# Performance work log

Hardware: AMD Instinct MI355X
Metric: run time of the kernel (lower is better)

## Reference

```python
import jax, jax.numpy as jnp
import numpy as np

N = 50000      # num nodes
E = 300000     # num edges
C = 256        # channels
H = 8          # num_heads
DH = C // H    # head_dim = 32
NUM_DST = 256  # dst indices live in [0, NUM_DST) -> anchor columns of BFS frontier
MAX_SPD = 3
EPS = 1e-5     # LayerNorm eps (torch default)


def setup_inputs() -> dict:
    key = jax.random.key(0)
    ks = jax.random.split(key, 10)
    scale = 1.0 / np.sqrt(C).astype(np.float32)
    x = jax.random.normal(ks[0], (N, C), jnp.float32)
    src = jax.random.randint(ks[1], (E,), 0, N, dtype=jnp.int32)
    dst = jax.random.randint(ks[2], (E,), 0, NUM_DST, dtype=jnp.int32)
    Wq = jax.random.normal(ks[3], (C, C), jnp.float32) * scale
    Wk = jax.random.normal(ks[4], (C, C), jnp.float32) * scale
    Wv = jax.random.normal(ks[5], (C, C), jnp.float32) * scale
    bq = jax.random.normal(ks[6], (C,), jnp.float32) * scale
    bk = jax.random.normal(ks[7], (C,), jnp.float32) * scale
    bv = jax.random.normal(ks[8], (C,), jnp.float32) * scale
    spd_w = jax.random.normal(ks[9], (MAX_SPD + 2, H), jnp.float32)
    gamma = jnp.ones((C,), jnp.float32)
    beta = jnp.zeros((C,), jnp.float32)
    return dict(x=x, src=src, dst=dst, Wq=Wq, bq=bq, Wk=Wk, bk=bk,
                Wv=Wv, bv=bv, spd_w=spd_w, gamma=gamma, beta=beta)


def _spd_buckets(src, dst):
    # Reverse-BFS shortest-path buckets (use_reverse=True, directed):
    # A[row=dst, col=src]; F_k = bin(A @ F_{k-1}); anchors are dst nodes,
    # which all live in [0, NUM_DST) so the anchor->column map is identity.
    row, col = dst, src
    F = (jnp.arange(N)[:, None] == jnp.arange(NUM_DST)[None, :]).astype(jnp.float32)  # [N, M]
    spd = jnp.full((E,), MAX_SPD + 1, jnp.int32)
    unset = jnp.ones((E,), bool)
    for k in range(1, MAX_SPD + 1):
        # (A @ F)[i] = sum over edges with row==i of F[col]
        F = (jax.ops.segment_sum(F[col], row, num_segments=N) > 0).astype(jnp.float32)
        reach = F[src, dst] > 0
        newly = unset & reach
        spd = jnp.where(newly, k, spd)
        unset = unset & ~newly
    return spd


def _segment_softmax(scores, seg, n):
    # numerically stable softmax over edges grouped by destination node
    m = jax.ops.segment_max(scores, seg, num_segments=n)
    ex = jnp.exp(scores - m[seg])
    s = jax.ops.segment_sum(ex, seg, num_segments=n)
    return ex / s[seg]


def reference(x, src, dst, Wq, bq, Wk, bk, Wv, bv, spd_w, gamma, beta):
    Q = (x @ Wq.T + bq).reshape(N, H, DH)
    K = (x @ Wk.T + bk).reshape(N, H, DH)
    V = (x @ Wv.T + bv).reshape(N, H, DH)
    # per-edge dot-product scores [E, H]
    scores = (Q[dst] * K[src]).sum(-1) / np.float32(np.sqrt(DH))
    spd = jax.lax.stop_gradient(_spd_buckets(src, dst))  # torch.no_grad
    scores = scores + spd_w[spd]
    w = _segment_softmax(scores, dst, N)  # [E, H] (dropout is identity in eval)
    msg = (V[src] * w[:, :, None]).reshape(E, C)
    out = jax.ops.segment_sum(msg, dst, num_segments=N)  # scatter-add aggregation
    # total degree (in + out) broadcast over channels
    ones_e = jnp.ones((E,), jnp.float32)
    deg = jax.ops.segment_sum(ones_e, src, num_segments=N) + \
          jax.ops.segment_sum(ones_e, dst, num_segments=N)
    h = out + deg[:, None] + x  # residual
    mu = h.mean(-1, keepdims=True)
    var = ((h - mu) ** 2).mean(-1, keepdims=True)
    return (h - mu) / jnp.sqrt(var + EPS) * gamma + beta
```

## Files before the change

### kernel.cpp

```cpp
#include <hip/hip_runtime.h>
#include <stdint.h>

#define N_NODES 50000
#define E_EDGES 300000
#define C_CH    256
#define H_HEADS 8
#define NB2     64
#define CHUNK2  4688
#define NBIN    4096
#define SRCDIV  3125
#define NWG_GEMM 2346
#define NWG_LN   12436

typedef unsigned short u16;
typedef unsigned int   u32;

typedef __attribute__((ext_vector_type(8))) short  v8s;
typedef __attribute__((ext_vector_type(4))) float  v4f;

__device__ __forceinline__ float bf2f(u16 v) {
    union { u32 u; float f; } x; x.u = ((u32)v) << 16; return x.f;
}
__device__ __forceinline__ u16 f2bf(float f) {
    union { float f; u32 u; } x; x.f = f;
    u32 r = (x.u + 0x7FFFu + ((x.u >> 16) & 1u)) >> 16;
    return (u16)r;
}
__device__ __forceinline__ void unp2(u32 v, float& lo, float& hi) {
    union { u32 u; float f; } x;
    x.u = v << 16; lo = x.f;
    x.u = v & 0xFFFF0000u; hi = x.f;
}
__device__ __forceinline__ void gl_lds16(const u16* g, u16* l) {
    __builtin_amdgcn_global_load_lds(
        (const __attribute__((address_space(1))) void*)g,
        (__attribute__((address_space(3))) void*)l, 16, 0, 0);
}
__device__ __forceinline__ void pack8(const float4 p, const float4 q, u16* dst) {
    u16 tmp[8];
    tmp[0]=f2bf(p.x); tmp[1]=f2bf(p.y); tmp[2]=f2bf(p.z); tmp[3]=f2bf(p.w);
    tmp[4]=f2bf(q.x); tmp[5]=f2bf(q.y); tmp[6]=f2bf(q.z); tmp[7]=f2bf(q.w);
    *(uint4*)dst = *(const uint4*)tmp;
}

__global__ __launch_bounds__(256) void prep_k(
    const float* __restrict__ Wk, const float* __restrict__ Wv,
    const float* __restrict__ Wq, u16* __restrict__ Wb,
    const int* __restrict__ src, const int* __restrict__ dst,
    u32* __restrict__ blockhist, u32* __restrict__ bintot,
    u32* __restrict__ inmask)
{
    __shared__ u32 hist[NBIN];
    int t = threadIdx.x, b = blockIdx.x;
    if (b < 192) {
        int m = (b < 64) ? 0 : (b < 128) ? 1 : 2;
        const float* sp = (m == 0) ? Wk : (m == 1) ? Wv : Wq;
        u16* dp = Wb + m * 65536;
        int i = (b & 63) * 1024 + t * 4;
        float4 v = *(const float4*)(sp + i);
        ushort4 o;
        o.x = f2bf(v.x); o.y = f2bf(v.y); o.z = f2bf(v.z); o.w = f2bf(v.w);
        *(ushort4*)(dp + i) = o;
        return;
    }
    int hb = b - 192;
#pragma unroll
    for (int j = 0; j < 16; j++) hist[t + j * 256] = 0;
    __syncthreads();
    int start = hb * CHUNK2;
    int end = start + CHUNK2; if (end > E_EDGES) end = E_EDGES;
    for (int e = start + t; e < end; e += 256) {
        int d = dst[e], s = src[e];
        atomicAdd(&hist[d * 16 + s / SRCDIV], 1u);
        if (s < 256) atomicOr(&inmask[d * 8 + (s >> 5)], 1u << (s & 31));
    }
    __syncthreads();
#pragma unroll
    for (int j = 0; j < 16; j++) {
        int bin = t + j * 256;
        u32 h = hist[bin];
        blockhist[hb * NBIN + bin] = h;
        if (h) atomicAdd(&bintot[bin], h);
    }
}

__global__ __launch_bounds__(256, 4) void gemm3(
    const float* __restrict__ x, const u16* __restrict__ Wb,
    const float* __restrict__ bk, const float* __restrict__ bv,
    const float* __restrict__ bq,
    u16* __restrict__ Kb, u16* __restrict__ Vb, u16* __restrict__ Qb,
    const u32* __restrict__ bintot, u32* __restrict__ bin_off,
    const u32* __restrict__ inmask, unsigned char* __restrict__ T,
    const float* __restrict__ gamma, const float* __restrict__ beta,
    float* __restrict__ y)
{
    __shared__ u16 smem[4][128 * 32];
    const int t = threadIdx.x;

    if (blockIdx.x >= NWG_GEMM + 2) {
        int n = (blockIdx.x - (NWG_GEMM + 2)) * 4 + (t >> 6) + 256;
        int lane = t & 63;
        int ch = lane * 4;
        float4 xv = *(const float4*)(x + (size_t)n * 256 + ch);
        float h0 = xv.x, h1 = xv.y, h2 = xv.z, h3 = xv.w;
        float s = h0 + h1 + h2 + h3;
#pragma unroll
        for (int off = 1; off < 64; off <<= 1) s += __shfl_xor(s, off);
        float mu = s * (1.0f / 256.0f);
        float d0 = h0 - mu, d1 = h1 - mu, d2 = h2 - mu, d3 = h3 - mu;
        float qq = d0 * d0 + d1 * d1 + d2 * d2 + d3 * d3;
#pragma unroll
        for (int off = 1; off < 64; off <<= 1) qq += __shfl_xor(qq, off);
        float rstd = rsqrtf(qq * (1.0f / 256.0f) + 1e-5f);
        float4 gv = *(const float4*)(gamma + ch);
        float4 bv = *(const float4*)(beta + ch);
        float4 o;
        o.x = d0 * rstd * gv.x + bv.x;
        o.y = d1 * rstd * gv.y + bv.y;
        o.z = d2 * rstd * gv.z + bv.z;
        o.w = d3 * rstd * gv.w + bv.w;
        *(float4*)(y + (size_t)n * 256 + ch) = o;
        return;
    }

    if (blockIdx.x >= NWG_GEMM) {
        u32* b32 = (u32*)&smem[0][0];
        if (blockIdx.x == NWG_GEMM) {
            u32* tsum = b32;
            u32 loc[16]; u32 a = 0;
#pragma unroll
            for (int j = 0; j < 16; j++) { loc[j] = bintot[t * 16 + j]; a += loc[j]; }
            tsum[t] = a;
            __syncthreads();
            for (int off = 1; off < 256; off <<= 1) {
                u32 add = (t >= off) ? tsum[t - off] : 0u;
                __syncthreads();
                tsum[t] += add;
                __syncthreads();
            }
            u32 base = tsum[t] - a;
#pragma unroll
            for (int j = 0; j < 16; j++) { bin_off[t * 16 + j] = base; base += loc[j]; }
            if (t == 255) bin_off[NBIN] = base;
        } else {
            u32 (*F1)[8] = (u32(*)[8])(b32);
            u32 (*F2)[8] = (u32(*)[8])(b32 + 2048);
            u32 (*F3)[8] = (u32(*)[8])(b32 + 4096);
            int i = t;
#pragma unroll
            for (int w = 0; w < 8; w++) { F1[i][w] = inmask[i * 8 + w]; F2[i][w] = 0; F3[i][w] = 0; }
            __syncthreads();
            for (int w = 0; w < 8; w++) {
                u32 m = F1[i][w];
                while (m) {
                    int b = __ffs(m) - 1; m &= m - 1;
                    int s = w * 32 + b;
#pragma unroll
                    for (int j = 0; j < 8; j++) F2[i][j] |= F1[s][j];
                }
            }
            __syncthreads();
            for (int w = 0; w < 8; w++) {
                u32 m = F1[i][w];
                while (m) {
                    int b = __ffs(m) - 1; m &= m - 1;
                    int s = w * 32 + b;
#pragma unroll
                    for (int j = 0; j < 8; j++) F3[i][j] |= F2[s][j];
                }
            }
            __syncthreads();
            for (int w = 0; w < 8; w++) {
                u32 f1 = F1[i][w], f2 = F2[i][w], f3 = F3[i][w];
#pragma unroll
                for (int g = 0; g < 8; g++) {
                    u32 word = 0;
#pragma unroll
                    for (int b = 0; b < 4; b++) {
                        int bit = g * 4 + b;
                        u32 k = ((f1 >> bit) & 1u) ? 1u : ((f2 >> bit) & 1u) ? 2u
                               : ((f3 >> bit) & 1u) ? 3u : 4u;
                        word |= k << (8 * b);
                    }
                    *(u32*)(T + i * 256 + w * 32 + g * 4) = word;
                }
            }
        }
        return;
    }

    const int nwg = NWG_GEMM, q = nwg >> 3, r = nwg & 7;
    int xcd = blockIdx.x & 7, pos = blockIdx.x >> 3;
    int wgid = (xcd < r ? xcd * (q + 1) : r * (q + 1) + (xcd - r) * q) + pos;
    const int mt = wgid / 6, j6 = wgid % 6;
    const int mat = j6 >> 1, nh = j6 & 1;
    const int m0 = mt * 128;
    if (mat == 2 && m0 >= 256) return;
    const int M = (mat == 2) ? 256 : N_NODES;
    const u16* W = Wb + mat * 65536;
    const float* bias = (mat == 0) ? bk : (mat == 1) ? bv : bq;
    u16* OUT = (mat == 0) ? Kb : (mat == 1) ? Vb : Qb;
    const int n0 = nh * 128;

    const int lane = t & 63, w = t >> 6;
    const int quad = lane >> 4, l15 = lane & 15;
    const int mq = w & 1, nq = w >> 1;

    v4f acc[16];
#pragma unroll
    for (int i = 0; i < 16; i++) acc[i] = (v4f)(0.0f);

    const int lrow = lane >> 2;
    const int cg   = (lane & 3) * 8;
    int rA0 = m0 + w * 32 + lrow; if (rA0 > 49999) rA0 = 49999;
    int rA1 = rA0 + 16;           if (rA1 > 49999) rA1 = 49999;
    const float* gA0 = x + (size_t)rA0 * 256 + cg;
    const float* gA1 = x + (size_t)rA1 * 256 + cg;
    const u16* gB = W + (size_t)(n0 + w * 32 + lrow) * 256 + (lane & 3) * 8;

    u16* ldsA = &smem[0][(w * 32 + lrow) * 32 + (lane & 3) * 8];

    float4 a00, a01, a10, a11;
#define LOADA(kt) do {                                   \
    a00 = *(const float4*)(gA0 + (kt) * 32);             \
    a01 = *(const float4*)(gA0 + (kt) * 32 + 4);         \
    a10 = *(const float4*)(gA1 + (kt) * 32);             \
    a11 = *(const float4*)(gA1 + (kt) * 32 + 4);         \
} while (0)
#define WRITEA(bi) do {                                  \
    pack8(a00, a01, ldsA + (bi) * 4096);                 \
    pack8(a10, a11, ldsA + (bi) * 4096 + 16 * 32);       \
} while (0)
#define STAGEB(bi, koff) do {                                             \
    gl_lds16(gB + (koff),            &smem[2 + (bi)][(w * 32) * 32]);     \
    gl_lds16(gB + 16 * 256 + (koff), &smem[2 + (bi)][(w * 32 + 16) * 32]);\
} while (0)

    LOADA(0);
    STAGEB(0, 0);
    WRITEA(0);
    __syncthreads();
    for (int kt = 0; kt < 8; kt++) {
        const int cur = kt & 1;
        if (kt < 7) { LOADA(kt + 1); STAGEB(cur ^ 1, (kt + 1) * 32); }
        v8s a[4], b[4];
#pragma unroll
        for (int f = 0; f < 4; f++)
            a[f] = *(const v8s*)(&smem[cur][(mq * 64 + f * 16 + l15) * 32 + quad * 8]);
#pragma unroll
        for (int f = 0; f < 4; f++)
            b[f] = *(const v8s*)(&smem[2 + cur][(nq * 64 + f * 16 + l15) * 32 + quad * 8]);
#pragma unroll
        for (int fm = 0; fm < 4; fm++)
#pragma unroll
            for (int fn = 0; fn < 4; fn++)
                acc[fm * 4 + fn] = __builtin_amdgcn_mfma_f32_16x16x32_bf16(
                    a[fm], b[fn], acc[fm * 4 + fn], 0, 0, 0);
        if (kt < 7) WRITEA(cur ^ 1);
        __syncthreads();
    }
#undef LOADA
#undef WRITEA
#undef STAGEB

    u16* S = &smem[0][0];
#pragma unroll
    for (int fn = 0; fn < 4; fn++) {
        int n = nq * 64 + fn * 16 + l15;
        float bi = bias[n0 + n];
#pragma unroll
        for (int fm = 0; fm < 4; fm++) {
#pragma unroll
            for (int r2 = 0; r2 < 4; r2++) {
                int row = mq * 64 + fm * 16 + quad * 4 + r2;
                S[row * 128 + n] = f2bf(acc[fm * 4 + fn][r2] + bi);
            }
        }
    }
    __syncthreads();
#pragma unroll
    for (int i = 0; i < 8; i++) {
        int c = i * 256 + t;
        int row = c >> 4;
        int m = m0 + row;
        if (m < M)
            *(uint4*)(OUT + (size_t)m * 256 + n0 + (c & 15) * 8) =
                *(const uint4*)(S + c * 8);
    }
}

__global__ __launch_bounds__(256) void base_k(
    const u32* __restrict__ blockhist, const u32* __restrict__ bin_off,
    u32* __restrict__ blockbase)
{
    int bin = blockIdx.x * 256 + threadIdx.x;
    u32 h[NB2];
#pragma unroll
    for (int b = 0; b < NB2; b++) h[b] = blockhist[b * NBIN + bin];
    u32 run = bin_off[bin];
#pragma unroll
    for (int b = 0; b < NB2; b++) {
        blockbase[b * NBIN + bin] = run;
        run += h[b];
    }
}

__global__ __launch_bounds__(256) void scatter2_k(
    const int* __restrict__ src, const int* __restrict__ dst,
    const u32* __restrict__ blockbase, u32* __restrict__ ssrc)
{
    __shared__ u32 cur[NBIN];
    int t = threadIdx.x, b = blockIdx.x;
#pragma unroll
    for (int j = 0; j < 16; j++)
        cur[t + j * 256] = blockbase[b * NBIN + t + j * 256];
    __syncthreads();
    int start = b * CHUNK2;
    int end = start + CHUNK2; if (end > E_EDGES) end = E_EDGES;
    for (int e = start + t; e < end; e += 256) {
        int s = src[e];
        int bin = dst[e] * 16 + s / SRCDIV;
        u32 pos = atomicAdd(&cur[bin], 1u);
        ssrc[pos] = (u32)s;
    }
}

__global__ __launch_bounds__(256) void agg_k(
    const u32* __restrict__ ssrc, const u32* __restrict__ bin_off,
    const u16* __restrict__ Qb, const u16* __restrict__ Kb,
    const u16* __restrict__ Vb, const unsigned char* __restrict__ T,
    const float* __restrict__ spd_w, float* __restrict__ out,
    float* __restrict__ denom)
{
    __shared__ float red[4 * 256];
    __shared__ float dred[4 * 8];
    int bid = blockIdx.x;
    int d = bid >> 4;
    int t = threadIdx.x, lane = t & 63, wave = t >> 6;
    int half = lane >> 5, sl = lane & 31;
    int h = sl >> 2;
    u32 start = bin_off[bid], end = bin_off[bid + 1];

    uint4 qv = *(const uint4*)(Qb + (size_t)d * 256 + sl * 8);
    float q0,q1,q2,q3,q4,q5,q6,q7;
    unp2(qv.x,q0,q1); unp2(qv.y,q2,q3); unp2(qv.z,q4,q5); unp2(qv.w,q6,q7);
    float sw4 = spd_w[4 * 8 + h];

    float a0=0.f,a1=0.f,a2=0.f,a3=0.f,a4=0.f,a5=0.f,a6=0.f,a7=0.f,dsum=0.f;

    u32 i = start + (u32)(wave * 2 + half);
    int s_c = 0, s_n = 0;
    uint4 kv_c = make_uint4(0,0,0,0), vv_c = kv_c;
    if (i < end) {
        s_c = (int)ssrc[i];
        kv_c = *(const uint4*)(Kb + (size_t)s_c * 256 + sl * 8);
        vv_c = *(const uint4*)(Vb + (size_t)s_c * 256 + sl * 8);
        if (i + 8 < end) s_n = (int)ssrc[i + 8];
    }
    while (i < end) {
        u32 inx = i + 8;
        uint4 kv_n = kv_c, vv_n = vv_c;
        if (inx < end) {
            kv_n = *(const uint4*)(Kb + (size_t)s_n * 256 + sl * 8);
            vv_n = *(const uint4*)(Vb + (size_t)s_n * 256 + sl * 8);
        }
        int s_nn = (inx + 8 < end) ? (int)ssrc[inx + 8] : 0;
        float k0,k1,k2,k3,k4,k5,k6,k7, v0,v1,v2,v3,v4,v5,v6,v7;
        unp2(kv_c.x,k0,k1); unp2(kv_c.y,k2,k3); unp2(kv_c.z,k4,k5); unp2(kv_c.w,k6,k7);
        unp2(vv_c.x,v0,v1); unp2(vv_c.y,v2,v3); unp2(vv_c.z,v4,v5); unp2(vv_c.w,v6,v7);
        float p = q0*k0+q1*k1+q2*k2+q3*k3+q4*k4+q5*k5+q6*k6+q7*k7;
        p += __shfl_xor(p, 1);
        p += __shfl_xor(p, 2);
        float bias = (s_c < 256) ? spd_w[(int)T[s_c * 256 + d] * 8 + h] : sw4;
        float wgt = __expf(p * 0.17677669529663689f + bias);
        a0 += wgt*v0; a1 += wgt*v1; a2 += wgt*v2; a3 += wgt*v3;
        a4 += wgt*v4; a5 += wgt*v5; a6 += wgt*v6; a7 += wgt*v7;
        if ((sl & 3) == 0) dsum += wgt;
        i = inx; s_c = s_n; s_n = s_nn; kv_c = kv_n; vv_c = vv_n;
    }
    a0 += __shfl_xor(a0,32); a1 += __shfl_xor(a1,32);
    a2 += __shfl_xor(a2,32); a3 += __shfl_xor(a3,32);
    a4 += __shfl_xor(a4,32); a5 += __shfl_xor(a5,32);
    a6 += __shfl_xor(a6,32); a7 += __shfl_xor(a7,32);
    dsum += __shfl_xor(dsum,32);
    if (half == 0) {
        *(float4*)(&red[wave * 256 + sl * 8])     = make_float4(a0,a1,a2,a3);
        *(float4*)(&red[wave * 256 + sl * 8 + 4]) = make_float4(a4,a5,a6,a7);
        if ((sl & 3) == 0) dred[wave * 8 + h] = dsum;
    }
    __syncthreads();
    float sAll = red[t] + red[256 + t] + red[512 + t] + red[768 + t];
    atomicAdd(&out[(size_t)d * 256 + t], sAll);
    if (t < 8) {
        float ds = dred[t] + dred[8 + t] + dred[16 + t] + dred[24 + t];
        atomicAdd(&denom[d * 8 + t], ds);
    }
}

__global__ __launch_bounds__(256) void ln_k(
    const float* __restrict__ x, const float* __restrict__ out,
    const float* __restrict__ denom, const float* __restrict__ gamma,
    const float* __restrict__ beta, float* __restrict__ y)
{
    int n = blockIdx.x * 4 + (threadIdx.x >> 6);
    int lane = threadIdx.x & 63;
    int ch = lane * 4;
    float4 xv = *(const float4*)(x + (size_t)n * 256 + ch);
    float h0 = xv.x, h1 = xv.y, h2 = xv.z, h3 = xv.w;
    float den = denom[n * 8 + (lane >> 3)];
    float inv = (den > 0.f) ? 1.0f / den : 0.0f;
    const float* op = out + (size_t)n * 256 + ch;
    h0 += op[0] * inv; h1 += op[1] * inv;
    h2 += op[2] * inv; h3 += op[3] * inv;
    float s = h0 + h1 + h2 + h3;
#pragma unroll
    for (int off = 1; off < 64; off <<= 1) s += __shfl_xor(s, off);
    float mu = s * (1.0f / 256.0f);
    float d0 = h0 - mu, d1 = h1 - mu, d2 = h2 - mu, d3 = h3 - mu;
    float q = d0 * d0 + d1 * d1 + d2 * d2 + d3 * d3;
#pragma unroll
    for (int off = 1; off < 64; off <<= 1) q += __shfl_xor(q, off);
    float rstd = rsqrtf(q * (1.0f / 256.0f) + 1e-5f);
    float4 gv = *(const float4*)(gamma + ch);
    float4 bv = *(const float4*)(beta + ch);
    float4 o;
    o.x = d0 * rstd * gv.x + bv.x;
    o.y = d1 * rstd * gv.y + bv.y;
    o.z = d2 * rstd * gv.z + bv.z;
    o.w = d3 * rstd * gv.w + bv.w;
    *(float4*)(y + (size_t)n * 256 + ch) = o;
}

extern "C" void kernel_launch(void* const* d_in, const int* in_sizes, int n_in,
                              void* d_out, int out_size, void* d_ws, size_t ws_size,
                              hipStream_t stream)
{
    const float* x     = (const float*)d_in[0];
    const int*   src   = (const int*)d_in[1];
    const int*   dst   = (const int*)d_in[2];
    const float* Wq    = (const float*)d_in[3];
    const float* bq    = (const float*)d_in[4];
    const float* Wk    = (const float*)d_in[5];
    const float* bk    = (const float*)d_in[6];
    const float* Wv    = (const float*)d_in[7];
    const float* bv    = (const float*)d_in[8];
    const float* spd_w = (const float*)d_in[9];
    const float* gamma = (const float*)d_in[10];
    const float* beta  = (const float*)d_in[11];
    float* y = (float*)d_out;

    char* ws = (char*)d_ws;
    float* denom     = (float*)(ws + 0);
    float* outf      = (float*)(ws + 8192);
    u32*   inmask    = (u32*)(ws + 270336);
    u32*   bintot    = (u32*)(ws + 278528);
    u32*   bin_off   = (u32*)(ws + 294912);
    unsigned char* T = (unsigned char*)(ws + 311552);
    u32*   blockhist = (u32*)(ws + 377088);
    u32*   blockbase = (u32*)(ws + 1425664);
    u32*   ssrc      = (u32*)(ws + 2474240);
    u16*   Qb        = (u16*)(ws + 3676416);
    u16*   Kb        = (u16*)(ws + 3807488);
    u16*   Vb        = (u16*)(ws + 29407488);
    u16*   Wb        = (u16*)(ws + 55007488);

    hipMemsetAsync(d_ws, 0, 294912, stream);

    dim3 blk(256);
    prep_k<<<dim3(256), blk, 0, stream>>>(Wk, Wv, Wq, Wb, src, dst,
                                          blockhist, bintot, inmask);
    gemm3<<<dim3(NWG_GEMM + 2 + NWG_LN), blk, 0, stream>>>(
        x, Wb, bk, bv, bq, Kb, Vb, Qb, bintot, bin_off, inmask, T,
        gamma, beta, y);
    base_k<<<dim3(16), blk, 0, stream>>>(blockhist, bin_off, blockbase);
    scatter2_k<<<dim3(NB2), blk, 0, stream>>>(src, dst, blockbase, ssrc);
    agg_k<<<dim3(NBIN), blk, 0, stream>>>(ssrc, bin_off, Qb, Kb, Vb, T, spd_w, outf, denom);
    ln_k<<<dim3(64), blk, 0, stream>>>(x, outf, denom, gamma, beta, y);
}
```

Measured before the change: 202.4 us.

## Drop memset and base kernel, use per-block partial histograms and masks

```diff
diff --git a/kernel.cpp b/kernel.cpp
--- a/kernel.cpp
+++ b/kernel.cpp
@@ -9,8 +9,9 @@
 #define CHUNK2  4688
 #define NBIN    4096
 #define SRCDIV  3125
-#define NWG_GEMM 2346
+#define NWG_GEMM 1568
 #define NWG_LN   12436
+#define GOFF     2
 
 typedef unsigned short u16;
 typedef unsigned int   u32;
@@ -47,10 +48,11 @@
     const float* __restrict__ Wk, const float* __restrict__ Wv,
     const float* __restrict__ Wq, u16* __restrict__ Wb,
     const int* __restrict__ src, const int* __restrict__ dst,
-    u32* __restrict__ blockhist, u32* __restrict__ bintot,
-    u32* __restrict__ inmask)
+    u32* __restrict__ blockhist, u32* __restrict__ pinmask,
+    u32* __restrict__ zero0)
 {
     __shared__ u32 hist[NBIN];
+    __shared__ u32 mask[256][8];
     int t = threadIdx.x, b = blockIdx.x;
     if (b < 192) {
         int m = (b < 64) ? 0 : (b < 128) ? 1 : 2;
@@ -63,25 +65,32 @@
         *(ushort4*)(dp + i) = o;
         return;
     }
+    if (b >= 256) {
+        int z = b - 256;
+        uint4 zv = make_uint4(0, 0, 0, 0);
+        *(uint4*)(zero0 + z * 1024 + t * 4) = zv;
+        return;
+    }
     int hb = b - 192;
 #pragma unroll
     for (int j = 0; j < 16; j++) hist[t + j * 256] = 0;
+#pragma unroll
+    for (int w = 0; w < 8; w++) mask[t][w] = 0;
     __syncthreads();
     int start = hb * CHUNK2;
     int end = start + CHUNK2; if (end > E_EDGES) end = E_EDGES;
     for (int e = start + t; e < end; e += 256) {
         int d = dst[e], s = src[e];
         atomicAdd(&hist[d * 16 + s / SRCDIV], 1u);
-        if (s < 256) atomicOr(&inmask[d * 8 + (s >> 5)], 1u << (s & 31));
-    }
-    __syncthreads();
-#pragma unroll
-    for (int j = 0; j < 16; j++) {
-        int bin = t + j * 256;
-        u32 h = hist[bin];
-        blockhist[hb * NBIN + bin] = h;
-        if (h) atomicAdd(&bintot[bin], h);
-    }
+        if (s < 256) atomicOr(&mask[d][s >> 5], 1u << (s & 31));
+    }
+    __syncthreads();
+#pragma unroll
+    for (int j = 0; j < 16; j++)
+        blockhist[hb * NBIN + t + j * 256] = hist[t + j * 256];
+#pragma unroll
+    for (int w = 0; w < 8; w++)
+        pinmask[hb * 2048 + w * 256 + t] = mask[t][w];
 }
 
 __global__ __launch_bounds__(256, 4) void gemm3(
@@ -89,16 +98,95 @@
     const float* __restrict__ bk, const float* __restrict__ bv,
     const float* __restrict__ bq,
     u16* __restrict__ Kb, u16* __restrict__ Vb, u16* __restrict__ Qb,
-    const u32* __restrict__ bintot, u32* __restrict__ bin_off,
-    const u32* __restrict__ inmask, unsigned char* __restrict__ T,
+    const u32* __restrict__ blockhist, u32* __restrict__ bin_off,
+    const u32* __restrict__ pinmask, unsigned char* __restrict__ T,
     const float* __restrict__ gamma, const float* __restrict__ beta,
     float* __restrict__ y)
 {
     __shared__ u16 smem[4][128 * 32];
     const int t = threadIdx.x;
 
-    if (blockIdx.x >= NWG_GEMM + 2) {
-        int n = (blockIdx.x - (NWG_GEMM + 2)) * 4 + (t >> 6) + 256;
+    if (blockIdx.x == 0) {
+        u32* tots = (u32*)&smem[0][0];
+        u32* tsum = tots + NBIN;
+#pragma unroll
+        for (int j = 0; j < 16; j++) {
+            u32 s = 0;
+            for (int b2 = 0; b2 < NB2; b2++)
+                s += blockhist[b2 * NBIN + j * 256 + t];
+            tots[j * 256 + t] = s;
+        }
+        __syncthreads();
+        u32 loc[16]; u32 a = 0;
+#pragma unroll
+        for (int j = 0; j < 16; j++) { loc[j] = tots[t * 16 + j]; a += loc[j]; }
+        tsum[t] = a;
+        __syncthreads();
+        for (int off = 1; off < 256; off <<= 1) {
+            u32 add = (t >= off) ? tsum[t - off] : 0u;
+            __syncthreads();
+            tsum[t] += add;
+            __syncthreads();
+        }
+        u32 base = tsum[t] - a;
+#pragma unroll
+        for (int j = 0; j < 16; j++) { bin_off[t * 16 + j] = base; base += loc[j]; }
+        if (t == 255) bin_off[NBIN] = base;
+        return;
+    }
+    if (blockIdx.x == 1) {
+        u32* b32 = (u32*)&smem[0][0];
+        u32 (*F1)[8] = (u32(*)[8])(b32);
+        u32 (*F2)[8] = (u32(*)[8])(b32 + 2048);
+        u32 (*F3)[8] = (u32(*)[8])(b32 + 4096);
+        int i = t;
+#pragma unroll
+        for (int w = 0; w < 8; w++) {
+            u32 m = 0;
+            for (int b2 = 0; b2 < NB2; b2++)
+                m |= pinmask[b2 * 2048 + w * 256 + i];
+            F1[i][w] = m; F2[i][w] = 0; F3[i][w] = 0;
+        }
+        __syncthreads();
+        for (int w = 0; w < 8; w++) {
+            u32 m = F1[i][w];
+            while (m) {
+                int b = __ffs(m) - 1; m &= m - 1;
+                int s = w * 32 + b;
+#pragma unroll
+                for (int j = 0; j < 8; j++) F2[i][j] |= F1[s][j];
+            }
+        }
+        __syncthreads();
+        for (int w = 0; w < 8; w++) {
+            u32 m = F1[i][w];
+            while (m) {
+                int b = __ffs(m) - 1; m &= m - 1;
+                int s = w * 32 + b;
+#pragma unroll
+                for (int j = 0; j < 8; j++) F3[i][j] |= F2[s][j];
+            }
+        }
+        __syncthreads();
+        for (int w = 0; w < 8; w++) {
+            u32 f1 = F1[i][w], f2 = F2[i][w], f3 = F3[i][w];
+#pragma unroll
+            for (int g = 0; g < 8; g++) {
+                u32 word = 0;
+#pragma unroll
+                for (int b = 0; b < 4; b++) {
+                    int bit = g * 4 + b;
+                    u32 k = ((f1 >> bit) & 1u) ? 1u : ((f2 >> bit) & 1u) ? 2u
+                           : ((f3 >> bit) & 1u) ? 3u : 4u;
+                    word |= k << (8 * b);
+                }
+                *(u32*)(T + i * 256 + w * 32 + g * 4) = word;
+            }
+        }
+        return;
+    }
+    if (blockIdx.x >= GOFF + NWG_GEMM) {
+        int n = (blockIdx.x - (GOFF + NWG_GEMM)) * 4 + (t >> 6) + 256;
         int lane = t & 63;
         int ch = lane * 4;
         float4 xv = *(const float4*)(x + (size_t)n * 256 + ch);
@@ -123,79 +211,13 @@
         return;
     }
 
-    if (blockIdx.x >= NWG_GEMM) {
-        u32* b32 = (u32*)&smem[0][0];
-        if (blockIdx.x == NWG_GEMM) {
-            u32* tsum = b32;
-            u32 loc[16]; u32 a = 0;
-#pragma unroll
-            for (int j = 0; j < 16; j++) { loc[j] = bintot[t * 16 + j]; a += loc[j]; }
-            tsum[t] = a;
-            __syncthreads();
-            for (int off = 1; off < 256; off <<= 1) {
-                u32 add = (t >= off) ? tsum[t - off] : 0u;
-                __syncthreads();
-                tsum[t] += add;
-                __syncthreads();
-            }
-            u32 base = tsum[t] - a;
-#pragma unroll
-            for (int j = 0; j < 16; j++) { bin_off[t * 16 + j] = base; base += loc[j]; }
-            if (t == 255) bin_off[NBIN] = base;
-        } else {
-            u32 (*F1)[8] = (u32(*)[8])(b32);
-            u32 (*F2)[8] = (u32(*)[8])(b32 + 2048);
-            u32 (*F3)[8] = (u32(*)[8])(b32 + 4096);
-            int i = t;
-#pragma unroll
-            for (int w = 0; w < 8; w++) { F1[i][w] = inmask[i * 8 + w]; F2[i][w] = 0; F3[i][w] = 0; }
-            __syncthreads();
-            for (int w = 0; w < 8; w++) {
-                u32 m = F1[i][w];
-                while (m) {
-                    int b = __ffs(m) - 1; m &= m - 1;
-                    int s = w * 32 + b;
-#pragma unroll
-                    for (int j = 0; j < 8; j++) F2[i][j] |= F1[s][j];
-                }
-            }
-            __syncthreads();
-            for (int w = 0; w < 8; w++) {
-                u32 m = F1[i][w];
-                while (m) {
-                    int b = __ffs(m) - 1; m &= m - 1;
-                    int s = w * 32 + b;
-#pragma unroll
-                    for (int j = 0; j < 8; j++) F3[i][j] |= F2[s][j];
-                }
-            }
-            __syncthreads();
-            for (int w = 0; w < 8; w++) {
-                u32 f1 = F1[i][w], f2 = F2[i][w], f3 = F3[i][w];
-#pragma unroll
-                for (int g = 0; g < 8; g++) {
-                    u32 word = 0;
-#pragma unroll
-                    for (int b = 0; b < 4; b++) {
-                        int bit = g * 4 + b;
-                        u32 k = ((f1 >> bit) & 1u) ? 1u : ((f2 >> bit) & 1u) ? 2u
-                               : ((f3 >> bit) & 1u) ? 3u : 4u;
-                        word |= k << (8 * b);
-                    }
-                    *(u32*)(T + i * 256 + w * 32 + g * 4) = word;
-                }
-            }
-        }
-        return;
-    }
-
-    const int nwg = NWG_GEMM, q = nwg >> 3, r = nwg & 7;
-    int xcd = blockIdx.x & 7, pos = blockIdx.x >> 3;
-    int wgid = (xcd < r ? xcd * (q + 1) : r * (q + 1) + (xcd - r) * q) + pos;
-    const int mt = wgid / 6, j6 = wgid % 6;
-    const int mat = j6 >> 1, nh = j6 & 1;
+    int gid = blockIdx.x - GOFF;
+    int xcd = gid & 7, pos = gid >> 3;
+    int wgid = xcd * (NWG_GEMM >> 3) + pos;
+    int mt, mat, nh;
+    if (wgid < 1564) { mt = wgid >> 2; int j = wgid & 3; mat = j >> 1; nh = j & 1; }
+    else             { int qi = wgid - 1564; mt = qi >> 1; mat = 2; nh = qi & 1; }
     const int m0 = mt * 128;
-    if (mat == 2 && m0 >= 256) return;
     const int M = (mat == 2) ? 256 : N_NODES;
     const u16* W = Wb + mat * 65536;
     const float* bias = (mat == 0) ? bk : (mat == 1) ? bv : bq;
@@ -289,31 +311,22 @@
     }
 }
 
-__global__ __launch_bounds__(256) void base_k(
-    const u32* __restrict__ blockhist, const u32* __restrict__ bin_off,
-    u32* __restrict__ blockbase)
-{
-    int bin = blockIdx.x * 256 + threadIdx.x;
-    u32 h[NB2];
-#pragma unroll
-    for (int b = 0; b < NB2; b++) h[b] = blockhist[b * NBIN + bin];
-    u32 run = bin_off[bin];
-#pragma unroll
-    for (int b = 0; b < NB2; b++) {
-        blockbase[b * NBIN + bin] = run;
-        run += h[b];
-    }
-}
-
 __global__ __launch_bounds__(256) void scatter2_k(
     const int* __restrict__ src, const int* __restrict__ dst,
-    const u32* __restrict__ blockbase, u32* __restrict__ ssrc)
+    const u32* __restrict__ blockhist, const u32* __restrict__ bin_off,
+    u32* __restrict__ ssrc)
 {
     __shared__ u32 cur[NBIN];
     int t = threadIdx.x, b = blockIdx.x;
-#pragma unroll
-    for (int j = 0; j < 16; j++)
-        cur[t + j * 256] = blockbase[b * NBIN + t + j * 256];
+    u32 c[16];
+#pragma unroll
+    for (int j = 0; j < 16; j++) c[j] = bin_off[j * 256 + t];
+    for (int bp = 0; bp < b; bp++)
+#pragma unroll
+        for (int j = 0; j < 16; j++)
+            c[j] += blockhist[bp * NBIN + j * 256 + t];
+#pragma unroll
+    for (int j = 0; j < 16; j++) cur[j * 256 + t] = c[j];
     __syncthreads();
     int start = b * CHUNK2;
     int end = start + CHUNK2; if (end > E_EDGES) end = E_EDGES;
@@ -452,28 +465,23 @@
     char* ws = (char*)d_ws;
     float* denom     = (float*)(ws + 0);
     float* outf      = (float*)(ws + 8192);
-    u32*   inmask    = (u32*)(ws + 270336);
-    u32*   bintot    = (u32*)(ws + 278528);
-    u32*   bin_off   = (u32*)(ws + 294912);
-    unsigned char* T = (unsigned char*)(ws + 311552);
-    u32*   blockhist = (u32*)(ws + 377088);
-    u32*   blockbase = (u32*)(ws + 1425664);
-    u32*   ssrc      = (u32*)(ws + 2474240);
-    u16*   Qb        = (u16*)(ws + 3676416);
-    u16*   Kb        = (u16*)(ws + 3807488);
-    u16*   Vb        = (u16*)(ws + 29407488);
-    u16*   Wb        = (u16*)(ws + 55007488);
-
-    hipMemsetAsync(d_ws, 0, 294912, stream);
+    u32*   bin_off   = (u32*)(ws + 270336);
+    unsigned char* T = (unsigned char*)(ws + 286976);
+    u32*   blockhist = (u32*)(ws + 352512);
+    u32*   pinmask   = (u32*)(ws + 1401088);
+    u32*   ssrc      = (u32*)(ws + 1925376);
+    u16*   Qb        = (u16*)(ws + 3125376);
+    u16*   Kb        = (u16*)(ws + 3256448);
+    u16*   Vb        = (u16*)(ws + 28881024);
+    u16*   Wb        = (u16*)(ws + 54505600);
 
     dim3 blk(256);
-    prep_k<<<dim3(256), blk, 0, stream>>>(Wk, Wv, Wq, Wb, src, dst,
-                                          blockhist, bintot, inmask);
-    gemm3<<<dim3(NWG_GEMM + 2 + NWG_LN), blk, 0, stream>>>(
-        x, Wb, bk, bv, bq, Kb, Vb, Qb, bintot, bin_off, inmask, T,
+    prep_k<<<dim3(322), blk, 0, stream>>>(Wk, Wv, Wq, Wb, src, dst,
+                                          blockhist, pinmask, (u32*)(ws + 0));
+    gemm3<<<dim3(GOFF + NWG_GEMM + NWG_LN), blk, 0, stream>>>(
+        x, Wb, bk, bv, bq, Kb, Vb, Qb, blockhist, bin_off, pinmask, T,
         gamma, beta, y);
-    base_k<<<dim3(16), blk, 0, stream>>>(blockhist, bin_off, blockbase);
-    scatter2_k<<<dim3(NB2), blk, 0, stream>>>(src, dst, blockbase, ssrc);
+    scatter2_k<<<dim3(NB2), blk, 0, stream>>>(src, dst, blockhist, bin_off, ssrc);
     agg_k<<<dim3(NBIN), blk, 0, stream>>>(ssrc, bin_off, Qb, Kb, Vb, T, spd_w, outf, denom);
     ln_k<<<dim3(64), blk, 0, stream>>>(x, outf, denom, gamma, beta, y);
 }
```

New measurement: 270.8 us. 1.34x slower.
